# Performance work log

Measured on AMD Instinct MI355X. Metric: run time of the kernel, lower is better.

## Reference

```python
import jax, jax.numpy as jnp
import numpy as np


def _conv1x1(x, w, b):
    # x: [B,C,H,W], w: [O,C], b: [O] -> [B,O,H,W]
    return jnp.einsum('oc,bchw->bohw', w, x) + b[None, :, None, None]


def setup_inputs() -> dict:
    key = jax.random.key(0)
    ks = jax.random.split(key, 9)
    B, C, O, H, W = 8, 192, 96, 64, 64
    s_in = 1.0 / np.sqrt(C)
    s_out = 1.0 / np.sqrt(O)
    return {
        'x': jax.random.normal(ks[0], (B, C, H, W), dtype=jnp.float32),
        'g_w': jax.random.normal(ks[1], (O, C), dtype=jnp.float32) * s_in,
        'g_b': jax.random.normal(ks[2], (O,), dtype=jnp.float32) * s_in,
        'theta_w': jax.random.normal(ks[3], (O, C), dtype=jnp.float32) * s_in,
        'theta_b': jax.random.normal(ks[4], (O,), dtype=jnp.float32) * s_in,
        'phi_w': jax.random.normal(ks[5], (O, C), dtype=jnp.float32) * s_in,
        'phi_b': jax.random.normal(ks[6], (O,), dtype=jnp.float32) * s_in,
        'W_w': jax.random.normal(ks[7], (C, O), dtype=jnp.float32) * s_out,
        'W_b': jax.random.normal(ks[8], (C,), dtype=jnp.float32) * s_out,
    }


def reference(x, g_w, g_b, theta_w, theta_b, phi_w, phi_b, W_w, W_b):
    B, C, H, W = x.shape
    O = g_w.shape[0]
    N = H * W
    # 1x1 conv projections, flattened to [B, O, N]
    g_x = _conv1x1(x, g_w, g_b).reshape(B, O, N)          # [B,O,N]
    theta_x = _conv1x1(x, theta_w, theta_b).reshape(B, O, N)
    phi_x = _conv1x1(x, phi_w, phi_b).reshape(B, O, N)
    # scores f1[b,n,m] = theta[:, :, n] . phi[:, :, m]
    f1 = jnp.einsum('bon,bom->bnm', theta_x, phi_x)       # [B,N,N]
    f_div_C = jax.nn.softmax(f1, axis=-1)
    # y[b,n,o] = sum_m f[b,n,m] * g[b,o,m]
    y = jnp.einsum('bnm,bom->bon', f_div_C, g_x)          # [B,O,N]
    y = y.reshape(B, O, H, W)
    W_y = _conv1x1(y, W_w, W_b)                           # [B,C,H,W]
    return W_y + x
```

## Files before the change

### kernel.cpp

```cpp
#include <hip/hip_runtime.h>

typedef unsigned short u16;
typedef unsigned int u32;
typedef float f32x4 __attribute__((ext_vector_type(4)));
typedef float f32x16 __attribute__((ext_vector_type(16)));
typedef _Float16 h16x8 __attribute__((ext_vector_type(8)));
typedef u32 u32x4 __attribute__((ext_vector_type(4)));
typedef u32 u32x2 __attribute__((ext_vector_type(2)));
typedef u16 u16x4 __attribute__((ext_vector_type(4)));

#define NB 8
#define CC 192
#define OO 96
#define NN 4096
#define NSPLIT 4
#define XPAD 200
#define LOG2E 1.4426950408889634f

static __device__ __forceinline__ u16 f2h(float f) {
  _Float16 h = (_Float16)f;
  return __builtin_bit_cast(u16, h);
}
static __device__ __forceinline__ void gl_lds16(const u16* g, u16* l) {
  __builtin_amdgcn_global_load_lds(
      (const __attribute__((address_space(1))) void*)g,
      (__attribute__((address_space(3))) void*)l, 16, 0, 0);
}
static __device__ __forceinline__ void plane_swap(u32& a, u32& b) {
  u32x2 r = __builtin_amdgcn_permlane32_swap(a, b, false, false);
  a = r[0]; b = r[1];
}
static __device__ __forceinline__ float half_combine_max(float x) {
  u32 a = __builtin_bit_cast(u32, x), b = a;
  plane_swap(a, b);
  return fmaxf(__builtin_bit_cast(float, a), __builtin_bit_cast(float, b));
}
static __device__ __forceinline__ float half_combine_sum(float x) {
  u32 a = __builtin_bit_cast(u32, x), b = a;
  plane_swap(a, b);
  return __builtin_bit_cast(float, a) + __builtin_bit_cast(float, b);
}
static __device__ __forceinline__ float max3f(float a, float b, float c) {
  return fmaxf(fmaxf(a, b), c);
}

__global__ __launch_bounds__(256) void proj_kernel(
    const float* __restrict__ x,
    const float* __restrict__ g_w, const float* __restrict__ g_b,
    const float* __restrict__ th_w, const float* __restrict__ th_b,
    const float* __restrict__ ph_w, const float* __restrict__ ph_b,
    u16* __restrict__ QB, u16* __restrict__ KA, u16* __restrict__ VA)
{
  __shared__ __align__(16) u16 Xs[64][XPAD];
  __shared__ __align__(16) u16 Ws[96][XPAD];
  const int b = blockIdx.y, n0 = blockIdx.x * 64, tid = threadIdx.x;
  const int lane = tid & 63, wv = tid >> 6, l15 = lane & 15, lg = lane >> 4;

  #pragma unroll
  for (int it = 0; it < 12; ++it) {
    int idx = tid + it * 256;
    int c = idx >> 4, q = idx & 15;
    float4 v = *(const float4*)(x + ((size_t)(b * CC + c)) * NN + n0 + q * 4);
    Xs[q * 4 + 0][c] = f2h(v.x); Xs[q * 4 + 1][c] = f2h(v.y);
    Xs[q * 4 + 2][c] = f2h(v.z); Xs[q * 4 + 3][c] = f2h(v.w);
  }

  for (int p = 0; p < 3; ++p) {
    const float* w    = (p == 0) ? th_w : (p == 1) ? ph_w : g_w;
    const float* bias = (p == 0) ? th_b : (p == 1) ? ph_b : g_b;
    const float scale = (p == 0) ? LOG2E : 1.0f;
    __syncthreads();
    #pragma unroll
    for (int it = 0; it < 18; ++it) {
      int idx = tid + it * 256;
      int r = idx / 48, q = idx % 48;
      float4 v = *(const float4*)(w + r * CC + q * 4);
      u16x4 hh; hh[0] = f2h(v.x * scale); hh[1] = f2h(v.y * scale);
      hh[2] = f2h(v.z * scale); hh[3] = f2h(v.w * scale);
      *(u16x4*)&Ws[r][q * 4] = hh;
    }
    __syncthreads();

    f32x4 acc[6];
    #pragma unroll
    for (int of = 0; of < 6; ++of) acc[of] = (f32x4){0.f, 0.f, 0.f, 0.f};
    #pragma unroll
    for (int ks = 0; ks < 6; ++ks) {
      h16x8 xa = *(const h16x8*)&Xs[wv * 16 + l15][ks * 32 + lg * 8];
      #pragma unroll
      for (int of = 0; of < 6; ++of) {
        h16x8 wf = *(const h16x8*)&Ws[of * 16 + l15][ks * 32 + lg * 8];
        if (p < 2) acc[of] = __builtin_amdgcn_mfma_f32_16x16x32_f16(xa, wf, acc[of], 0, 0, 0);
        else       acc[of] = __builtin_amdgcn_mfma_f32_16x16x32_f16(wf, xa, acc[of], 0, 0, 0);
      }
    }

    if (p < 2) {
      u16* dst = (p == 0) ? QB : KA;
      #pragma unroll
      for (int of = 0; of < 6; ++of) {
        int o = of * 16 + l15;
        float bo = bias[o] * scale;
        int kch = of * 2 + (l15 >> 3);
        #pragma unroll
        for (int r = 0; r < 4; ++r) {
          int n = n0 + wv * 16 + lg * 4 + r;
          int idx = (b * 128 + (n >> 5)) * 3072 + (kch * 32 + (n & 31)) * 8 + (o & 7);
          dst[idx] = f2h(acc[of][r] + bo);
        }
      }
    } else {
      #pragma unroll
      for (int of = 0; of < 6; ++of) {
        #pragma unroll
        for (int r = 0; r < 4; ++r) {
          int o = of * 16 + lg * 4 + r;
          int m = n0 + wv * 16 + l15;
          int idx = (b * 256 + (m >> 4)) * 1536 +
                    (((o >> 5) * 2 + ((m >> 3) & 1)) * 32 + (o & 31)) * 8 + (m & 7);
          VA[idx] = f2h(acc[of][r] + bias[o]);
        }
      }
    }
  }
}

__global__ __launch_bounds__(256, 2) void attn_kernel(
    const u16* __restrict__ QB, const u16* __restrict__ KA,
    const u16* __restrict__ VA, u16* __restrict__ yP, float* __restrict__ ml)
{
  __shared__ __align__(16) u16 Ks[2][6144];
  __shared__ __align__(16) u16 Vs[2][6144];
  const int b   = blockIdx.x;
  const int qt  = blockIdx.y;
  const int sp  = blockIdx.z;
  const int tid = threadIdx.x;
  const int lane = tid & 63;
  const int wv  = tid >> 6;
  const int l31 = lane & 31;
  const int h   = lane >> 5;

  const int t_start = 16 * sp;
  const int t_end   = 16 * (sp + 1);

  const int ncA = qt * 8 + wv * 2;
  const int ncB = ncA + 1;
  const u16* qbA = QB + (size_t)(b * 128 + ncA) * 3072;
  const u16* qbB = QB + (size_t)(b * 128 + ncB) * 3072;
  h16x8 qfA[6], qfB[6];
  #pragma unroll
  for (int ks = 0; ks < 6; ++ks) {
    qfA[ks] = *(const h16x8*)(qbA + ((ks * 2 + h) * 32 + l31) * 8);
    qfB[ks] = *(const h16x8*)(qbB + ((ks * 2 + h) * 32 + l31) * 8);
  }

  const u16* KAb = KA + (size_t)b * (128 * 3072);
  const u16* VAb = VA + (size_t)b * (256 * 1536);

  f32x16 accA[3], accB[3];
  #pragma unroll
  for (int ob = 0; ob < 3; ++ob)
    #pragma unroll
    for (int i = 0; i < 16; ++i) { accA[ob][i] = 0.f; accB[ob][i] = 0.f; }
  float mA = -3.0e38f, lA = 0.f;
  float mB = -3.0e38f, lB = 0.f;

  {
    const u16* gk = KAb + (size_t)t_start * 6144;
    const u16* gv = VAb + (size_t)t_start * 6144;
    #pragma unroll
    for (int i = 0; i < 3; ++i) gl_lds16(gk + tid * 8 + i * 2048, &Ks[0][tid * 8 + i * 2048]);
    #pragma unroll
    for (int i = 0; i < 3; ++i) gl_lds16(gv + tid * 8 + i * 2048, &Vs[0][tid * 8 + i * 2048]);
  }

  for (int t = t_start; t < t_end; ++t) {
    const int bf = (t - t_start) & 1;
    if (t + 1 < t_end) {
      const u16* gk = KAb + (size_t)(t + 1) * 6144;
      const u16* gv = VAb + (size_t)(t + 1) * 6144;
      #pragma unroll
      for (int i = 0; i < 3; ++i) gl_lds16(gk + tid * 8 + i * 2048, &Ks[bf ^ 1][tid * 8 + i * 2048]);
      #pragma unroll
      for (int i = 0; i < 3; ++i) gl_lds16(gv + tid * 8 + i * 2048, &Vs[bf ^ 1][tid * 8 + i * 2048]);
      asm volatile("s_waitcnt vmcnt(6)" ::: "memory");
    } else {
      asm volatile("s_waitcnt vmcnt(0)" ::: "memory");
    }
    __builtin_amdgcn_s_barrier();
    __builtin_amdgcn_sched_barrier(0);

    #pragma unroll
    for (int c = 0; c < 2; ++c) {
      const u16* kc = &Ks[bf][c * 3072];
      const u16* vc = &Vs[bf][c * 3072];
      f32x16 SA, SB;
      #pragma unroll
      for (int i = 0; i < 16; ++i) { SA[i] = 0.f; SB[i] = 0.f; }
      #pragma unroll
      for (int ks = 0; ks < 6; ++ks) {
        h16x8 kf = *(const h16x8*)(kc + ((ks * 2 + h) * 32 + l31) * 8);
        SA = __builtin_amdgcn_mfma_f32_32x32x16_f16(kf, qfA[ks], SA, 0, 0, 0);
        SB = __builtin_amdgcn_mfma_f32_32x32x16_f16(kf, qfB[ks], SB, 0, 0, 0);
      }

      u32 pkA[8];
      {
        float t0 = max3f(SA[0], SA[1], SA[2]),   t1 = max3f(SA[3], SA[4], SA[5]);
        float t2 = max3f(SA[6], SA[7], SA[8]),   t3 = max3f(SA[9], SA[10], SA[11]);
        float t4 = max3f(SA[12], SA[13], SA[14]);
        float pmax = half_combine_max(fmaxf(max3f(t0, t1, t2), max3f(t3, t4, SA[15])));
        if (__ballot(pmax > mA + 11.5416f)) {
          float mn = fmaxf(mA, pmax);
          float sc = exp2f(mA - mn);
          mA = mn; lA *= sc;
          #pragma unroll
          for (int ob = 0; ob < 3; ++ob)
            #pragma unroll
            for (int i = 0; i < 16; ++i) accA[ob][i] *= sc;
        }
        #pragma unroll
        for (int i = 0; i < 16; ++i) SA[i] = exp2f(SA[i] - mA);
        #pragma unroll
        for (int i = 0; i < 8; ++i)
          pkA[i] = __builtin_bit_cast(u32, __builtin_amdgcn_cvt_pkrtz(SA[2 * i], SA[2 * i + 1]));
        #pragma unroll
        for (int st = 8; st >= 1; st >>= 1)
          #pragma unroll
          for (int i = 0; i < 8; ++i) if (i < st) SA[i] += SA[i + st];
        lA += half_combine_sum(SA[0]);
        plane_swap(pkA[0], pkA[2]); plane_swap(pkA[1], pkA[3]);
        plane_swap(pkA[4], pkA[6]); plane_swap(pkA[5], pkA[7]);
      }
      u32 pkB[8];
      {
        float t0 = max3f(SB[0], SB[1], SB[2]),   t1 = max3f(SB[3], SB[4], SB[5]);
        float t2 = max3f(SB[6], SB[7], SB[8]),   t3 = max3f(SB[9], SB[10], SB[11]);
        float t4 = max3f(SB[12], SB[13], SB[14]);
        float pmax = half_combine_max(fmaxf(max3f(t0, t1, t2), max3f(t3, t4, SB[15])));
        if (__ballot(pmax > mB + 11.5416f)) {
          float mn = fmaxf(mB, pmax);
          float sc = exp2f(mB - mn);
          mB = mn; lB *= sc;
          #pragma unroll
          for (int ob = 0; ob < 3; ++ob)
            #pragma unroll
            for (int i = 0; i < 16; ++i) accB[ob][i] *= sc;
        }
        #pragma unroll
        for (int i = 0; i < 16; ++i) SB[i] = exp2f(SB[i] - mB);
        #pragma unroll
        for (int i = 0; i < 8; ++i)
          pkB[i] = __builtin_bit_cast(u32, __builtin_amdgcn_cvt_pkrtz(SB[2 * i], SB[2 * i + 1]));
        #pragma unroll
        for (int st = 8; st >= 1; st >>= 1)
          #pragma unroll
          for (int i = 0; i < 8; ++i) if (i < st) SB[i] += SB[i + st];
        lB += half_combine_sum(SB[0]);
        plane_swap(pkB[0], pkB[2]); plane_swap(pkB[1], pkB[3]);
        plane_swap(pkB[4], pkB[6]); plane_swap(pkB[5], pkB[7]);
      }
      u32x4 a0 = {pkA[0], pkA[1], pkA[2], pkA[3]}, a1 = {pkA[4], pkA[5], pkA[6], pkA[7]};
      u32x4 b0 = {pkB[0], pkB[1], pkB[2], pkB[3]}, b1 = {pkB[4], pkB[5], pkB[6], pkB[7]};
      h16x8 pfA[2] = {__builtin_bit_cast(h16x8, a0), __builtin_bit_cast(h16x8, a1)};
      h16x8 pfB[2] = {__builtin_bit_cast(h16x8, b0), __builtin_bit_cast(h16x8, b1)};

      #pragma unroll
      for (int s2 = 0; s2 < 2; ++s2) {
        #pragma unroll
        for (int ob = 0; ob < 3; ++ob) {
          h16x8 vf = *(const h16x8*)(vc + (((s2 * 3 + ob) * 2 + h) * 32 + l31) * 8);
          accA[ob] = __builtin_amdgcn_mfma_f32_32x32x16_f16(vf, pfA[s2], accA[ob], 0, 0, 0);
          accB[ob] = __builtin_amdgcn_mfma_f32_32x32x16_f16(vf, pfB[s2], accB[ob], 0, 0, 0);
        }
      }
    }
    __builtin_amdgcn_s_barrier();
    __builtin_amdgcn_sched_barrier(0);
  }

  #pragma unroll
  for (int qq = 0; qq < 2; ++qq) {
    const f32x16* acc = qq ? accB : accA;
    float mR = qq ? mB : mA, lR = qq ? lB : lA;
    float inv = 1.0f / lR;
    int nglob = (qq ? ncB : ncA) * 32 + l31;
    u16* yp = yP + (((size_t)sp * NB + b) * NN + nglob) * OO;
    #pragma unroll
    for (int ob = 0; ob < 3; ++ob) {
      #pragma unroll
      for (int rq = 0; rq < 4; ++rq) {
        int o0 = ob * 32 + rq * 8 + h * 4;
        u32 w0 = __builtin_bit_cast(u32,
            __builtin_amdgcn_cvt_pkrtz(acc[ob][rq * 4 + 0] * inv, acc[ob][rq * 4 + 1] * inv));
        u32 w1 = __builtin_bit_cast(u32,
            __builtin_amdgcn_cvt_pkrtz(acc[ob][rq * 4 + 2] * inv, acc[ob][rq * 4 + 3] * inv));
        uint2 pr; pr.x = w0; pr.y = w1;
        *(uint2*)&yp[o0] = pr;
      }
    }
    if (h == 0) {
      float2 v2; v2.x = mR; v2.y = lR;
      *(float2*)&ml[(((size_t)sp * NB + b) * NN + nglob) * 2] = v2;
    }
  }
}

#define YPAD 104
__global__ __launch_bounds__(256) void outproj_kernel(
    const float* __restrict__ x, const float* __restrict__ Ww,
    const float* __restrict__ Wb, const u16* __restrict__ yP,
    const float* __restrict__ ml, float* __restrict__ out)
{
  __shared__ __align__(16) u16 Wws[CC][YPAD];
  __shared__ __align__(16) u16 Ys[64][YPAD];
  const int b = blockIdx.y, n0 = blockIdx.x * 64, tid = threadIdx.x;
  const int lane = tid & 63, wv = tid >> 6, l15 = lane & 15, lg = lane >> 4;
  const size_t SB = (size_t)NB * NN;

  #pragma unroll
  for (int it = 0; it < 18; ++it) {
    int idx = tid + it * 256;
    int r = idx / 24, q = idx % 24;
    float4 v = *(const float4*)(Ww + r * OO + q * 4);
    u16x4 hh; hh[0] = f2h(v.x); hh[1] = f2h(v.y); hh[2] = f2h(v.z); hh[3] = f2h(v.w);
    *(u16x4*)&Wws[r][q * 4] = hh;
  }
  #pragma unroll
  for (int it = 0; it < 3; ++it) {
    int idx = tid + it * 256;
    int n = idx / 12, q = idx % 12;
    size_t bn = (size_t)b * NN + n0 + n;
    float mm[NSPLIT], ll[NSPLIT];
    float M = -3.0e38f;
    #pragma unroll
    for (int s = 0; s < NSPLIT; ++s) {
      mm[s] = ml[((size_t)s * SB + bn) * 2];
      ll[s] = ml[((size_t)s * SB + bn) * 2 + 1];
      M = fmaxf(M, mm[s]);
    }
    float wsum = 0.f, w[NSPLIT];
    #pragma unroll
    for (int s = 0; s < NSPLIT; ++s) { w[s] = ll[s] * exp2f(mm[s] - M); wsum += w[s]; }
    float rinv = 1.0f / wsum;
    #pragma unroll
    for (int s = 0; s < NSPLIT; ++s) w[s] *= rinv;
    float accv[8];
    #pragma unroll
    for (int e = 0; e < 8; ++e) accv[e] = 0.f;
    #pragma unroll
    for (int s = 0; s < NSPLIT; ++s) {
      h16x8 ys = *(const h16x8*)(yP + ((size_t)s * SB + bn) * OO + q * 8);
      #pragma unroll
      for (int e = 0; e < 8; ++e) accv[e] += w[s] * (float)ys[e];
    }
    u32x4 packed;
    #pragma unroll
    for (int e = 0; e < 4; ++e)
      packed[e] = __builtin_bit_cast(u32,
          __builtin_amdgcn_cvt_pkrtz(accv[2 * e], accv[2 * e + 1]));
    *(u32x4*)&Ys[n][q * 8] = packed;
  }
  __syncthreads();

  f32x4 acc[12];
  #pragma unroll
  for (int cf = 0; cf < 12; ++cf) acc[cf] = (f32x4){0.f, 0.f, 0.f, 0.f};
  #pragma unroll
  for (int ks = 0; ks < 3; ++ks) {
    h16x8 yb = *(const h16x8*)&Ys[wv * 16 + l15][ks * 32 + lg * 8];
    #pragma unroll
    for (int cf = 0; cf < 12; ++cf) {
      h16x8 wa = *(const h16x8*)&Wws[cf * 16 + l15][ks * 32 + lg * 8];
      acc[cf] = __builtin_amdgcn_mfma_f32_16x16x32_f16(wa, yb, acc[cf], 0, 0, 0);
    }
  }
  #pragma unroll
  for (int cf = 0; cf < 12; ++cf) {
    #pragma unroll
    for (int r = 0; r < 4; ++r) {
      int c = cf * 16 + lg * 4 + r;
      size_t off = ((size_t)(b * CC + c)) * NN + n0 + wv * 16 + l15;
      out[off] = acc[cf][r] + x[off] + Wb[c];
    }
  }
}

extern "C" void kernel_launch(void* const* d_in, const int* in_sizes, int n_in,
                              void* d_out, int out_size, void* d_ws, size_t ws_size,
                              hipStream_t stream) {
  const float* x    = (const float*)d_in[0];
  const float* g_w  = (const float*)d_in[1];
  const float* g_b  = (const float*)d_in[2];
  const float* th_w = (const float*)d_in[3];
  const float* th_b = (const float*)d_in[4];
  const float* ph_w = (const float*)d_in[5];
  const float* ph_b = (const float*)d_in[6];
  const float* W_w  = (const float*)d_in[7];
  const float* W_b  = (const float*)d_in[8];
  float* out = (float*)d_out;

  char* ws = (char*)d_ws;
  const size_t projB = (size_t)NB * NN * OO * sizeof(u16);
  u16* QB   = (u16*)ws;
  u16* KA   = (u16*)(ws + projB);
  u16* VA   = (u16*)(ws + 2 * projB);
  u16* yP   = (u16*)(ws + 3 * projB);
  float* ml = (float*)(ws + (3 + NSPLIT) * projB);

  dim3 blk(256);
  dim3 gproj(64, NB);
  hipLaunchKernelGGL(proj_kernel, gproj, blk, 0, stream,
                     x, g_w, g_b, th_w, th_b, ph_w, ph_b, QB, KA, VA);
  dim3 gattn(NB, 16, NSPLIT);
  hipLaunchKernelGGL(attn_kernel, gattn, blk, 0, stream, QB, KA, VA, yP, ml);
  dim3 gout(64, NB);
  hipLaunchKernelGGL(outproj_kernel, gout, blk, 0, stream, x, W_w, W_b, yP, ml, out);
}
```

Measured before the change: 108.8 us.

## Shrink attention blocks to two waves, single-buffer K/V, use raw exp

The attention kernel now runs 128-thread blocks of two waves, each covering four query tiles instead of eight, and launches twice as many blocks. K/V staging in LDS drops from double to single buffering, so each step loads synchronously and waits on vmcnt(0). The goal is smaller LDS and block footprint, giving more resident blocks per CU to hide latency instead of in-block prefetch. exp2f is replaced by an inline v_exp_f32 to skip range-handling code. This loses load/compute overlap within a block and doubles K/V global traffic across query tiles.

Result: faster. 97.84 us (-10.1%).

```diff
diff --git a/kernel.cpp b/kernel.cpp
--- a/kernel.cpp
+++ b/kernel.cpp
@@ -25,6 +25,11 @@
   __builtin_amdgcn_global_load_lds(
       (const __attribute__((address_space(1))) void*)g,
       (__attribute__((address_space(3))) void*)l, 16, 0, 0);
+}
+static __device__ __forceinline__ float exp2_raw(float x) {
+  float r;
+  asm("v_exp_f32 %0, %1" : "=v"(r) : "v"(x));
+  return r;
 }
 static __device__ __forceinline__ void plane_swap(u32& a, u32& b) {
   u32x2 r = __builtin_amdgcn_permlane32_swap(a, b, false, false);
@@ -125,12 +130,12 @@
   }
 }
 
-__global__ __launch_bounds__(256, 2) void attn_kernel(
+__global__ __launch_bounds__(128, 2) void attn_kernel(
     const u16* __restrict__ QB, const u16* __restrict__ KA,
     const u16* __restrict__ VA, u16* __restrict__ yP, float* __restrict__ ml)
 {
-  __shared__ __align__(16) u16 Ks[2][6144];
-  __shared__ __align__(16) u16 Vs[2][6144];
+  __shared__ __align__(16) u16 Ks[6144];
+  __shared__ __align__(16) u16 Vs[6144];
   const int b   = blockIdx.x;
   const int qt  = blockIdx.y;
   const int sp  = blockIdx.z;
@@ -143,7 +148,7 @@
   const int t_start = 16 * sp;
   const int t_end   = 16 * (sp + 1);
 
-  const int ncA = qt * 8 + wv * 2;
+  const int ncA = qt * 4 + wv * 2;
   const int ncB = ncA + 1;
   const u16* qbA = QB + (size_t)(b * 128 + ncA) * 3072;
   const u16* qbB = QB + (size_t)(b * 128 + ncB) * 3072;
@@ -154,8 +159,8 @@
     qfB[ks] = *(const h16x8*)(qbB + ((ks * 2 + h) * 32 + l31) * 8);
   }
 
-  const u16* KAb = KA + (size_t)b * (128 * 3072);
-  const u16* VAb = VA + (size_t)b * (256 * 1536);
+  const u16* gk = KA + (size_t)b * (128 * 3072) + (size_t)t_start * 6144;
+  const u16* gv = VA + (size_t)b * (256 * 1536) + (size_t)t_start * 6144;
 
   f32x16 accA[3], accB[3];
   #pragma unroll
@@ -165,35 +170,20 @@
   float mA = -3.0e38f, lA = 0.f;
   float mB = -3.0e38f, lB = 0.f;
 
-  {
-    const u16* gk = KAb + (size_t)t_start * 6144;
-    const u16* gv = VAb + (size_t)t_start * 6144;
-    #pragma unroll
-    for (int i = 0; i < 3; ++i) gl_lds16(gk + tid * 8 + i * 2048, &Ks[0][tid * 8 + i * 2048]);
-    #pragma unroll
-    for (int i = 0; i < 3; ++i) gl_lds16(gv + tid * 8 + i * 2048, &Vs[0][tid * 8 + i * 2048]);
-  }
-
   for (int t = t_start; t < t_end; ++t) {
-    const int bf = (t - t_start) & 1;
-    if (t + 1 < t_end) {
-      const u16* gk = KAb + (size_t)(t + 1) * 6144;
-      const u16* gv = VAb + (size_t)(t + 1) * 6144;
-      #pragma unroll
-      for (int i = 0; i < 3; ++i) gl_lds16(gk + tid * 8 + i * 2048, &Ks[bf ^ 1][tid * 8 + i * 2048]);
-      #pragma unroll
-      for (int i = 0; i < 3; ++i) gl_lds16(gv + tid * 8 + i * 2048, &Vs[bf ^ 1][tid * 8 + i * 2048]);
-      asm volatile("s_waitcnt vmcnt(6)" ::: "memory");
-    } else {
-      asm volatile("s_waitcnt vmcnt(0)" ::: "memory");
-    }
+    #pragma unroll
+    for (int i = 0; i < 6; ++i) gl_lds16(gk + tid * 8 + i * 1024, &Ks[tid * 8 + i * 1024]);
+    #pragma unroll
+    for (int i = 0; i < 6; ++i) gl_lds16(gv + tid * 8 + i * 1024, &Vs[tid * 8 + i * 1024]);
+    gk += 6144; gv += 6144;
+    asm volatile("s_waitcnt vmcnt(0)" ::: "memory");
     __builtin_amdgcn_s_barrier();
     __builtin_amdgcn_sched_barrier(0);
 
     #pragma unroll
     for (int c = 0; c < 2; ++c) {
-      const u16* kc = &Ks[bf][c * 3072];
-      const u16* vc = &Vs[bf][c * 3072];
+      const u16* kc = &Ks[c * 3072];
+      const u16* vc = &Vs[c * 3072];
       f32x16 SA, SB;
       #pragma unroll
       for (int i = 0; i < 16; ++i) { SA[i] = 0.f; SB[i] = 0.f; }
@@ -212,7 +202,7 @@
         float pmax = half_combine_max(fmaxf(max3f(t0, t1, t2), max3f(t3, t4, SA[15])));
         if (__ballot(pmax > mA + 11.5416f)) {
           float mn = fmaxf(mA, pmax);
-          float sc = exp2f(mA - mn);
+          float sc = exp2_raw(mA - mn);
           mA = mn; lA *= sc;
           #pragma unroll
           for (int ob = 0; ob < 3; ++ob)
@@ -220,7 +210,7 @@
             for (int i = 0; i < 16; ++i) accA[ob][i] *= sc;
         }
         #pragma unroll
-        for (int i = 0; i < 16; ++i) SA[i] = exp2f(SA[i] - mA);
+        for (int i = 0; i < 16; ++i) SA[i] = exp2_raw(SA[i] - mA);
         #pragma unroll
         for (int i = 0; i < 8; ++i)
           pkA[i] = __builtin_bit_cast(u32, __builtin_amdgcn_cvt_pkrtz(SA[2 * i], SA[2 * i + 1]));
@@ -240,7 +230,7 @@
         float pmax = half_combine_max(fmaxf(max3f(t0, t1, t2), max3f(t3, t4, SB[15])));
         if (__ballot(pmax > mB + 11.5416f)) {
           float mn = fmaxf(mB, pmax);
-          float sc = exp2f(mB - mn);
+          float sc = exp2_raw(mB - mn);
           mB = mn; lB *= sc;
           #pragma unroll
           for (int ob = 0; ob < 3; ++ob)
@@ -248,7 +238,7 @@
             for (int i = 0; i < 16; ++i) accB[ob][i] *= sc;
         }
         #pragma unroll
-        for (int i = 0; i < 16; ++i) SB[i] = exp2f(SB[i] - mB);
+        for (int i = 0; i < 16; ++i) SB[i] = exp2_raw(SB[i] - mB);
         #pragma unroll
         for (int i = 0; i < 8; ++i)
           pkB[i] = __builtin_bit_cast(u32, __builtin_amdgcn_cvt_pkrtz(SB[2 * i], SB[2 * i + 1]));
@@ -276,7 +266,6 @@
       }
     }
     __builtin_amdgcn_s_barrier();
-    __builtin_amdgcn_sched_barrier(0);
   }
 
   #pragma unroll
@@ -408,12 +397,11 @@
   u16* yP   = (u16*)(ws + 3 * projB);
   float* ml = (float*)(ws + (3 + NSPLIT) * projB);
 
-  dim3 blk(256);
   dim3 gproj(64, NB);
-  hipLaunchKernelGGL(proj_kernel, gproj, blk, 0, stream,
+  hipLaunchKernelGGL(proj_kernel, gproj, dim3(256), 0, stream,
                      x, g_w, g_b, th_w, th_b, ph_w, ph_b, QB, KA, VA);
-  dim3 gattn(NB, 16, NSPLIT);
-  hipLaunchKernelGGL(attn_kernel, gattn, blk, 0, stream, QB, KA, VA, yP, ml);
+  dim3 gattn(NB, 32, NSPLIT);
+  hipLaunchKernelGGL(attn_kernel, gattn, dim3(128), 0, stream, QB, KA, VA, yP, ml);
   dim3 gout(64, NB);
-  hipLaunchKernelGGL(outproj_kernel, gout, blk, 0, stream, x, W_w, W_b, yP, ml, out);
-}
+  hipLaunchKernelGGL(outproj_kernel, gout, dim3(256), 0, stream, x, W_w, W_b, yP, ml, out);
+}
```
